# Kernel optimization log

Measured on AMD Instinct MI355X. Metric: run time of the kernel, lower is better.

## Reference

```python
import jax, jax.numpy as jnp
import numpy as np

B, S, E, H = 2, 2048, 1024, 16
D = E // H

def setup_inputs() -> dict:
    key = jax.random.key(0)
    ks = jax.random.split(key, 5)
    return {
        "hidden_states": jax.random.normal(ks[0], (B, S, E), dtype=jnp.float32),
        "c_attn_w": jax.random.normal(ks[1], (E, 3 * E), dtype=jnp.float32) * 0.02,
        "c_attn_b": jax.random.normal(ks[2], (3 * E,), dtype=jnp.float32) * 0.02,
        "c_proj_w": jax.random.normal(ks[3], (E, E), dtype=jnp.float32) * 0.02,
        "c_proj_b": jax.random.normal(ks[4], (E,), dtype=jnp.float32) * 0.02,
    }

def reference(hidden_states, c_attn_w, c_attn_b, c_proj_w, c_proj_b):
    x = hidden_states                      # [B, S, E]
    b, s, _ = x.shape
    w_q, w_k, w_v = jnp.split(c_attn_w, 3, axis=1)   # each [E, E]
    q_b, k_b, v_b = jnp.split(c_attn_b, 3, axis=0)   # each [E]

    # value projection
    v = x @ w_v + v_b                                        # [B,S,E]
    v = v.reshape(b, s, H, D).transpose(0, 2, 1, 3)          # [B,H,S,D]

    # fused query: ((x Wq + qb) Wk^T + kb)
    q = (x @ w_q + q_b) @ w_k.T + k_b                        # [B,S,E]
    qh = q.reshape(b, s, H, D).transpose(0, 2, 1, 3)         # [B,H,S,D]

    # key side is RAW hidden states split per head
    kh = x.reshape(b, s, H, D).transpose(0, 2, 1, 3)         # [B,H,S,D]

    scale = 1.0 / jnp.float32(D) ** 0.5
    scores = jnp.einsum("bhqd,bhkd->bhqk",
                        qh.astype(jnp.float32),
                        kh.astype(jnp.float32)) * scale       # [B,H,S,S] fp32

    causal = jnp.tril(jnp.ones((s, s), dtype=bool))
    mask_value = jnp.finfo(jnp.float32).min
    scores = jnp.where(causal[None, None], scores, mask_value)

    probs = jax.nn.softmax(scores, axis=-1).astype(v.dtype)  # [B,H,S,S]

    out = jnp.einsum("bhqk,bhkd->bhqd", probs, v)            # [B,H,S,D]
    out = out.transpose(0, 2, 1, 3).reshape(b, s, E)         # [B,S,E]
    out = out @ c_proj_w + c_proj_b
    return out
```

## Files before the change

kernel.cpp:

```cpp
#include <hip/hip_runtime.h>

typedef __attribute__((ext_vector_type(8))) __bf16 bf16x8;
typedef __attribute__((ext_vector_type(4))) __bf16 bf16x4;
typedef __attribute__((ext_vector_type(4))) float f32x4;

typedef __attribute__((address_space(1))) void as1_void;
typedef __attribute__((address_space(3))) void as3_void;

__device__ __forceinline__ void gl_lds16(const void* g, void* l) {
    __builtin_amdgcn_global_load_lds((const as1_void*)g, (as3_void*)l, 16, 0, 0);
}

__device__ __forceinline__ const bf16x8* swz(const __bf16* base, int row, int chunk) {
    return (const bf16x8*)((const char*)base + row * 128 + ((chunk ^ (row & 7)) * 16));
}

#define QSCALE (0.125f * 1.44269504f)

__global__ __launch_bounds__(256) void prep_kernel(
    const float* __restrict__ x, const float* __restrict__ caw,
    const float* __restrict__ cab, const float* __restrict__ cpw,
    __bf16* __restrict__ xb, __bf16* __restrict__ wvt,
    __bf16* __restrict__ wkn, __bf16* __restrict__ wqn,
    __bf16* __restrict__ wpt, float* __restrict__ bqv)
{
    __shared__ float tile[32 * 33];
    int bid = blockIdx.x;
    int tid = threadIdx.x;
    if (bid < 1024) {
        int nt = bid >> 5, kt = bid & 31;
        int tx = tid & 31, ty = tid >> 5;
        int n0 = nt * 32, k0 = kt * 32;
#pragma unroll
        for (int i = 0; i < 4; ++i)
            tile[(ty + i * 8) * 33 + tx] = caw[(long)(k0 + ty + i * 8) * 3072 + 2048 + n0 + tx];
        __syncthreads();
#pragma unroll
        for (int i = 0; i < 4; ++i)
            wvt[(long)(n0 + ty + i * 8) * 1024 + k0 + tx] = (__bf16)tile[tx * 33 + ty + i * 8];
    } else if (bid < 2048) {
        int v = bid - 1024;
        int nt = v >> 5, kt = v & 31;
        int tx = tid & 31, ty = tid >> 5;
        int n0 = nt * 32, k0 = kt * 32;
#pragma unroll
        for (int i = 0; i < 4; ++i)
            tile[(ty + i * 8) * 33 + tx] = cpw[(long)(k0 + ty + i * 8) * 1024 + n0 + tx];
        __syncthreads();
#pragma unroll
        for (int i = 0; i < 4; ++i)
            wpt[(long)(n0 + ty + i * 8) * 1024 + k0 + tx] = (__bf16)tile[tx * 33 + ty + i * 8];
    } else if (bid < 3072) {
        int e = (bid - 2048) * 1024 + tid * 4;
        int n = e >> 10, k = e & 1023;
        float4 f = *(const float4*)(caw + (long)n * 3072 + 1024 + k);
        bf16x4 o = {(__bf16)f.x, (__bf16)f.y, (__bf16)f.z, (__bf16)f.w};
        *(bf16x4*)(wkn + e) = o;
    } else if (bid < 4096) {
        int e = (bid - 3072) * 1024 + tid * 4;
        int n = e >> 10, k = e & 1023;
        float4 f = *(const float4*)(caw + (long)n * 3072 + k);
        bf16x4 o = {(__bf16)f.x, (__bf16)f.y, (__bf16)f.z, (__bf16)f.w};
        *(bf16x4*)(wqn + e) = o;
    } else if (bid < 8192) {
        long e = (long)(bid - 4096) * 1024 + tid * 4;
        float4 f = *(const float4*)(x + e);
        bf16x4 o = {(__bf16)f.x, (__bf16)f.y, (__bf16)f.z, (__bf16)f.w};
        *(bf16x4*)(xb + e) = o;
    } else {
        int k = bid - 8192;
        int wave = tid >> 6, lane = tid & 63;
        float qv[16];
#pragma unroll
        for (int u = 0; u < 4; ++u) {
            float4 q4 = *(const float4*)(cab + u * 256 + lane * 4);
            qv[u * 4 + 0] = q4.x; qv[u * 4 + 1] = q4.y;
            qv[u * 4 + 2] = q4.z; qv[u * 4 + 3] = q4.w;
        }
        for (int i = 0; i < 16; ++i) {
            int n = k * 64 + wave * 16 + i;
            float s = 0.f;
#pragma unroll
            for (int u = 0; u < 4; ++u) {
                float4 w4 = *(const float4*)(caw + (long)n * 3072 + 1024 + u * 256 + lane * 4);
                s += w4.x * qv[u * 4 + 0] + w4.y * qv[u * 4 + 1]
                   + w4.z * qv[u * 4 + 2] + w4.w * qv[u * 4 + 3];
            }
#pragma unroll
            for (int off = 1; off < 64; off <<= 1) s += __shfl_xor(s, off);
            if (lane == 0) bqv[n] = (s + cab[1024 + n]) * QSCALE;
        }
        if (tid < 64) bqv[1024 + k * 64 + tid] = cab[2048 + k * 64 + tid];
    }
}

template <bool BF16OUT, int BN>
__global__ __launch_bounds__(256) void gemm_bt(
    const __bf16* __restrict__ A, int lda,
    const __bf16* __restrict__ B, int ldb,
    const float* __restrict__ bias,
    void* __restrict__ C, int ldc, int K, float oscale)
{
    constexpr int NT = BN / 32;
    __shared__ __bf16 As[128 * 64];
    __shared__ __bf16 Bs[BN * 64];
    const int tid = threadIdx.x;
    const int lane = tid & 63;
    const int wave = tid >> 6;
    const int quad = lane >> 4, l16 = lane & 15;
    const long m0 = (long)blockIdx.y * 128;
    const long n0 = (long)blockIdx.x * BN;
    const int wm = (wave >> 1) * 64, wn = (wave & 1) * (BN / 2);

    f32x4 acc[4][NT] = {};

    for (int k0 = 0; k0 < K; k0 += 64) {
#pragma unroll
        for (int c = tid; c < (128 + BN) * 8; c += 256) {
            int row = c >> 3, cc = (c & 7) ^ (row & 7);
            if (row < 128)
                gl_lds16(A + (m0 + row) * lda + k0 + cc * 8, As + c * 8);
            else
                gl_lds16(B + (n0 + row - 128) * ldb + k0 + cc * 8, Bs + (c - 1024) * 8);
        }
        __syncthreads();
#pragma unroll
        for (int kk = 0; kk < 2; ++kk) {
            bf16x8 af[4], bfr[NT];
#pragma unroll
            for (int i = 0; i < 4; ++i)
                af[i] = *swz(As, wm + i * 16 + l16, kk * 4 + quad);
#pragma unroll
            for (int j = 0; j < NT; ++j)
                bfr[j] = *swz(Bs, wn + j * 16 + l16, kk * 4 + quad);
#pragma unroll
            for (int i = 0; i < 4; ++i)
#pragma unroll
                for (int j = 0; j < NT; ++j)
                    acc[i][j] = __builtin_amdgcn_mfma_f32_16x16x32_bf16(af[i], bfr[j], acc[i][j], 0, 0, 0);
        }
        __syncthreads();
    }
#pragma unroll
    for (int i = 0; i < 4; ++i) {
        long row = m0 + wm + i * 16 + quad * 4;
#pragma unroll
        for (int j = 0; j < NT; ++j) {
            int col = (int)n0 + wn + j * 16 + l16;
            float bb = bias ? bias[col] : 0.f;
#pragma unroll
            for (int r = 0; r < 4; ++r) {
                float v = (acc[i][j][r] + bb) * oscale;
                if (BF16OUT)
                    ((__bf16*)C)[(row + r) * ldc + col] = (__bf16)v;
                else
                    ((float*)C)[(row + r) * ldc + col] = v;
            }
        }
    }
}

__global__ __launch_bounds__(256) void gemm_qv(
    const __bf16* __restrict__ A,
    const __bf16* __restrict__ B,
    const float* __restrict__ bias,
    __bf16* __restrict__ Qout,
    __bf16* __restrict__ VTout)
{
    __shared__ __bf16 smem[128 * 136];
    __bf16* As = smem;
    __bf16* Bs = smem + 8192;
    const int tid = threadIdx.x;
    const int lane = tid & 63;
    const int wave = tid >> 6;
    const int quad = lane >> 4, l16 = lane & 15;
    const long m0 = (long)blockIdx.y * 128;
    const long n0 = (long)blockIdx.x * 128;
    const int wm = (wave >> 1) * 64, wn = (wave & 1) * 64;

    f32x4 acc[4][4] = {};

    for (int k0 = 0; k0 < 1024; k0 += 64) {
#pragma unroll
        for (int c = tid; c < 2048; c += 256) {
            int row = c >> 3, cc = (c & 7) ^ (row & 7);
            if (row < 128)
                gl_lds16(A + (m0 + row) * 1024 + k0 + cc * 8, As + c * 8);
            else
                gl_lds16(B + (n0 + row - 128) * 1024 + k0 + cc * 8, Bs + (c - 1024) * 8);
        }
        __syncthreads();
#pragma unroll
        for (int kk = 0; kk < 2; ++kk) {
            bf16x8 af[4], bfr[4];
#pragma unroll
            for (int i = 0; i < 4; ++i)
                af[i] = *swz(As, wm + i * 16 + l16, kk * 4 + quad);
#pragma unroll
            for (int j = 0; j < 4; ++j)
                bfr[j] = *swz(Bs, wn + j * 16 + l16, kk * 4 + quad);
#pragma unroll
            for (int i = 0; i < 4; ++i)
#pragma unroll
                for (int j = 0; j < 4; ++j)
                    acc[i][j] = __builtin_amdgcn_mfma_f32_16x16x32_bf16(af[i], bfr[j], acc[i][j], 0, 0, 0);
        }
        __syncthreads();
    }

    if (n0 < 1024) {
#pragma unroll
        for (int i = 0; i < 4; ++i) {
            long row = m0 + wm + i * 16 + quad * 4;
#pragma unroll
            for (int j = 0; j < 4; ++j) {
                int col = (int)n0 + wn + j * 16 + l16;
                float bb = bias[col];
#pragma unroll
                for (int r = 0; r < 4; ++r)
                    Qout[(row + r) * 1024 + col] = (__bf16)(acc[i][j][r] + bb);
            }
        }
    } else {
        __syncthreads();
#pragma unroll
        for (int i = 0; i < 4; ++i) {
#pragma unroll
            for (int j = 0; j < 4; ++j) {
                int col = (int)n0 + wn + j * 16 + l16;
                float bb = bias[col];
                bf16x4 v;
#pragma unroll
                for (int r = 0; r < 4; ++r) v[r] = (__bf16)(acc[i][j][r] + bb);
                *(bf16x4*)(smem + (wn + j * 16 + l16) * 136 + wm + i * 16 + quad * 4) = v;
            }
        }
        __syncthreads();
        const int d0 = (int)n0 - 1024;
        const int bb = (int)(m0 >> 11);
        const int sl = (int)(m0 & 2047);
#pragma unroll
        for (int pass = 0; pass < 16; ++pass) {
            int idx = pass * 256 + tid;
            int n = idx >> 5;
            int mc = (idx & 31) * 4;
            bf16x4 v = *(const bf16x4*)(smem + n * 136 + mc);
            *(bf16x4*)(VTout + ((long)(bb * 1024 + d0 + n)) * 2048 + sl + mc) = v;
        }
    }
}

__global__ __launch_bounds__(256, 2) void attn_kernel(
    const __bf16* __restrict__ Q,
    const __bf16* __restrict__ Xb,
    const __bf16* __restrict__ VT,
    __bf16* __restrict__ O)
{
    __shared__ __bf16 Ks[2 * 8192];
    __shared__ __bf16 Vs[2 * 8192];
    __shared__ __bf16 Ps[4 * 2048];
    const int tid = threadIdx.x;
    const int lane = tid & 63;
    const int wave = tid >> 6;
    const int group = wave >> 1;
    const int w2 = wave & 1;
    const int quad = lane >> 4, l16 = lane & 15;
    const int qa = blockIdx.y;
    const int qb = 31 - qa;
    const int qt = group ? qb : qa;
    const int bh = blockIdx.x;
    const int b = bh >> 4, h = bh & 15;
    const long rowbase = (long)b * 2048;

    const int i0 = tid, i1 = tid + 256;
    const int r0 = i0 >> 3, c0 = ((i0 & 7) ^ (r0 & 7)) * 8;
    const int r1 = i1 >> 3, c1 = ((i1 & 7) ^ (r1 & 7)) * 8;

    bf16x8 ones;
#pragma unroll
    for (int i = 0; i < 8; ++i) ones[i] = (__bf16)1.0f;

    bf16x8 qfr[2][2];
#pragma unroll
    for (int qg = 0; qg < 2; ++qg) {
        const __bf16* qp = Q + (rowbase + qt * 64 + w2 * 32 + qg * 16 + l16) * 1024 + h * 64 + quad * 8;
        qfr[qg][0] = *(const bf16x8*)(qp);
        qfr[qg][1] = *(const bf16x8*)(qp + 32);
    }

    const __bf16* kp0 = Xb + (rowbase + r0) * 1024 + h * 64 + c0;
    const __bf16* kp1 = Xb + (rowbase + r1) * 1024 + h * 64 + c1;
    const __bf16* vp0 = VT + ((long)(b * 1024 + h * 64 + r0)) * 2048 + c0;
    const __bf16* vp1 = VT + ((long)(b * 1024 + h * 64 + r1)) * 2048 + c1;

    auto stage_tile = [&](int j, int buf, int sub) {
        __bf16* kd = Ks + buf * 8192 + sub * 4096;
        __bf16* vd = Vs + buf * 8192 + sub * 4096;
        gl_lds16(kp0 + (long)j * 65536, kd + i0 * 8);
        gl_lds16(kp1 + (long)j * 65536, kd + i1 * 8);
        gl_lds16(vp0 + j * 64, vd + i0 * 8);
        gl_lds16(vp1 + j * 64, vd + i1 * 8);
    };
    stage_tile(0, 0, 0);
    stage_tile(1, 0, 1);

    const int nouter = (qb + 2) >> 1;

    f32x4 oacc[4][2] = {};
    f32x4 lacc[2] = {};
    __bf16* Pw = Ps + wave * 2048;

    for (int jj = 0; jj < nouter; ++jj) {
        __syncthreads();
        if (jj + 1 < nouter) {
            stage_tile(2 * jj + 2, (jj + 1) & 1, 0);
            stage_tile(2 * jj + 3, (jj + 1) & 1, 1);
        }

#pragma unroll
        for (int sub = 0; sub < 2; ++sub) {
            const int j = 2 * jj + sub;
            if (j > qt) continue;
            const __bf16* Kb = Ks + (jj & 1) * 8192 + sub * 4096;
            const __bf16* Vb = Vs + (jj & 1) * 8192 + sub * 4096;

            bf16x8 kf[2][4], vf[2][4];
#pragma unroll
            for (int kk = 0; kk < 2; ++kk)
#pragma unroll
                for (int kt = 0; kt < 4; ++kt) {
                    kf[kk][kt] = *swz(Kb, kt * 16 + l16, kk * 4 + quad);
                    vf[kk][kt] = *swz(Vb, kt * 16 + l16, kk * 4 + quad);
                }

            f32x4 sacc[4][2] = {};
#pragma unroll
            for (int kk = 0; kk < 2; ++kk)
#pragma unroll
                for (int kt = 0; kt < 4; ++kt)
#pragma unroll
                    for (int qg = 0; qg < 2; ++qg)
                        sacc[kt][qg] = __builtin_amdgcn_mfma_f32_16x16x32_bf16(
                            kf[kk][kt], qfr[qg][kk], sacc[kt][qg], 0, 0, 0);

            if (j == qt) {
#pragma unroll
                for (int kt = 0; kt < 4; ++kt)
#pragma unroll
                    for (int qg = 0; qg < 2; ++qg) {
                        const int qloc = w2 * 32 + qg * 16 + l16;
                        bf16x4 pk;
#pragma unroll
                        for (int r = 0; r < 4; ++r) {
                            float s = sacc[kt][qg][r];
                            if (kt * 16 + quad * 4 + r > qloc) s = -1e30f;
                            pk[r] = (__bf16)exp2f(s);
                        }
                        *(bf16x4*)((char*)Pw + (qg * 16 + l16) * 128 +
                                   (((kt * 2 + (quad >> 1)) ^ (l16 & 7)) * 16) + (quad & 1) * 8) = pk;
                    }
            } else {
#pragma unroll
                for (int kt = 0; kt < 4; ++kt)
#pragma unroll
                    for (int qg = 0; qg < 2; ++qg) {
                        bf16x4 pk;
#pragma unroll
                        for (int r = 0; r < 4; ++r)
                            pk[r] = (__bf16)exp2f(sacc[kt][qg][r]);
                        *(bf16x4*)((char*)Pw + (qg * 16 + l16) * 128 +
                                   (((kt * 2 + (quad >> 1)) ^ (l16 & 7)) * 16) + (quad & 1) * 8) = pk;
                    }
            }

#pragma unroll
            for (int kk = 0; kk < 2; ++kk) {
                bf16x8 pf[2];
#pragma unroll
                for (int qg = 0; qg < 2; ++qg) {
                    pf[qg] = *swz(Pw, qg * 16 + l16, kk * 4 + quad);
                    lacc[qg] = __builtin_amdgcn_mfma_f32_16x16x32_bf16(ones, pf[qg], lacc[qg], 0, 0, 0);
                }
#pragma unroll
                for (int dt = 0; dt < 4; ++dt)
#pragma unroll
                    for (int qg = 0; qg < 2; ++qg)
                        oacc[dt][qg] = __builtin_amdgcn_mfma_f32_16x16x32_bf16(
                            vf[kk][dt], pf[qg], oacc[dt][qg], 0, 0, 0);
            }
        }
    }

#pragma unroll
    for (int qg = 0; qg < 2; ++qg) {
        float inv = 1.0f / lacc[qg][0];
        long row = rowbase + qt * 64 + w2 * 32 + qg * 16 + l16;
#pragma unroll
        for (int dt = 0; dt < 4; ++dt) {
            bf16x4 ov;
#pragma unroll
            for (int r = 0; r < 4; ++r) ov[r] = (__bf16)(oacc[dt][qg][r] * inv);
            *(bf16x4*)(O + row * 1024 + h * 64 + dt * 16 + quad * 4) = ov;
        }
    }
}

extern "C" void kernel_launch(void* const* d_in, const int* in_sizes, int n_in,
                              void* d_out, int out_size, void* d_ws, size_t ws_size,
                              hipStream_t stream) {
    const float* x   = (const float*)d_in[0];
    const float* caw = (const float*)d_in[1];
    const float* cab = (const float*)d_in[2];
    const float* cpw = (const float*)d_in[3];
    const float* cpb = (const float*)d_in[4];

    char* p = (char*)d_ws;
    auto alloc = [&](size_t bytes) {
        void* r = (void*)p;
        p += (bytes + 255) & ~(size_t)255;
        return r;
    };
    __bf16* xb    = (__bf16*)alloc(4096UL * 1024 * 2);
    __bf16* mtb   = (__bf16*)alloc(1024UL * 1024 * 2);
    __bf16* wvt   = (__bf16*)alloc(1024UL * 1024 * 2);
    __bf16* wkn   = (__bf16*)alloc(1024UL * 1024 * 2);
    __bf16* wqn   = (__bf16*)alloc(1024UL * 1024 * 2);
    __bf16* wpt   = (__bf16*)alloc(1024UL * 1024 * 2);
    float*  bqv   = (float*) alloc(2048UL * 4);
    __bf16* qbuf  = (__bf16*)alloc(4096UL * 1024 * 2);
    __bf16* vt    = (__bf16*)alloc(2048UL * 2048 * 2);
    __bf16* attn  = (__bf16*)alloc(4096UL * 1024 * 2);

    prep_kernel<<<8208, 256, 0, stream>>>(x, caw, cab, cpw, xb, wvt, wkn, wqn, wpt, bqv);

    gemm_bt<true, 32><<<dim3(32, 8), 256, 0, stream>>>(wkn, 1024, wqn, 1024, nullptr,
                                                       (void*)mtb, 1024, 1024, QSCALE);
    gemm_qv<<<dim3(16, 32), 256, 0, stream>>>(xb, mtb, bqv, qbuf, vt);
    attn_kernel<<<dim3(32, 16), 256, 0, stream>>>(qbuf, xb, vt, attn);
    gemm_bt<false, 64><<<dim3(16, 32), 256, 0, stream>>>(attn, 1024, wpt, 1024, cpb,
                                                         d_out, 1024, 1024, 1.0f);
    (void)in_sizes; (void)n_in; (void)out_size; (void)ws_size;
}
```

Baseline: 191.8 us.

## Load V fragments directly from global memory and stage only K through LDS

The attention loop now processes one 64-key tile per iteration instead of two. Only K is double-buffered in LDS, while V fragments are read per wave straight from global memory into registers. The aim is to shrink LDS use and drop the V LDS round trip, with occupancy now left to the compiler by removing the launch-bounds minimum. The cost is that every wave issues its own global V loads, which duplicates traffic across waves, and those loads are exposed to memory latency with no prefetch. There is also one barrier per tile instead of one per two tiles.

```diff
diff --git a/kernel.cpp b/kernel.cpp
--- a/kernel.cpp
+++ b/kernel.cpp
@@ -250,14 +250,13 @@
     }
 }
 
-__global__ __launch_bounds__(256, 2) void attn_kernel(
+__global__ __launch_bounds__(256) void attn_kernel(
     const __bf16* __restrict__ Q,
     const __bf16* __restrict__ Xb,
     const __bf16* __restrict__ VT,
     __bf16* __restrict__ O)
 {
-    __shared__ __bf16 Ks[2 * 8192];
-    __shared__ __bf16 Vs[2 * 8192];
+    __shared__ __bf16 Ks[2 * 4096];
     __shared__ __bf16 Ps[4 * 2048];
     const int tid = threadIdx.x;
     const int lane = tid & 63;
@@ -290,104 +289,93 @@
 
     const __bf16* kp0 = Xb + (rowbase + r0) * 1024 + h * 64 + c0;
     const __bf16* kp1 = Xb + (rowbase + r1) * 1024 + h * 64 + c1;
-    const __bf16* vp0 = VT + ((long)(b * 1024 + h * 64 + r0)) * 2048 + c0;
-    const __bf16* vp1 = VT + ((long)(b * 1024 + h * 64 + r1)) * 2048 + c1;
-
-    auto stage_tile = [&](int j, int buf, int sub) {
-        __bf16* kd = Ks + buf * 8192 + sub * 4096;
-        __bf16* vd = Vs + buf * 8192 + sub * 4096;
+    const __bf16* vbase = VT + ((long)(b * 1024 + h * 64 + l16)) * 2048 + quad * 8;
+
+    auto stage_k = [&](int j, int buf) {
+        __bf16* kd = Ks + buf * 4096;
         gl_lds16(kp0 + (long)j * 65536, kd + i0 * 8);
         gl_lds16(kp1 + (long)j * 65536, kd + i1 * 8);
-        gl_lds16(vp0 + j * 64, vd + i0 * 8);
-        gl_lds16(vp1 + j * 64, vd + i1 * 8);
     };
-    stage_tile(0, 0, 0);
-    stage_tile(1, 0, 1);
-
-    const int nouter = (qb + 2) >> 1;
+    stage_k(0, 0);
 
     f32x4 oacc[4][2] = {};
     f32x4 lacc[2] = {};
     __bf16* Pw = Ps + wave * 2048;
 
-    for (int jj = 0; jj < nouter; ++jj) {
-        __syncthreads();
-        if (jj + 1 < nouter) {
-            stage_tile(2 * jj + 2, (jj + 1) & 1, 0);
-            stage_tile(2 * jj + 3, (jj + 1) & 1, 1);
-        }
-
-#pragma unroll
-        for (int sub = 0; sub < 2; ++sub) {
-            const int j = 2 * jj + sub;
-            if (j > qt) continue;
-            const __bf16* Kb = Ks + (jj & 1) * 8192 + sub * 4096;
-            const __bf16* Vb = Vs + (jj & 1) * 8192 + sub * 4096;
-
-            bf16x8 kf[2][4], vf[2][4];
-#pragma unroll
-            for (int kk = 0; kk < 2; ++kk)
-#pragma unroll
-                for (int kt = 0; kt < 4; ++kt) {
-                    kf[kk][kt] = *swz(Kb, kt * 16 + l16, kk * 4 + quad);
-                    vf[kk][kt] = *swz(Vb, kt * 16 + l16, kk * 4 + quad);
+    for (int j = 0; j <= qb; ++j) {
+        __syncthreads();
+        if (j < qb) stage_k(j + 1, (j + 1) & 1);
+        if (j > qt) continue;
+        const __bf16* Kb = Ks + (j & 1) * 4096;
+
+        bf16x8 vf[2][4];
+#pragma unroll
+        for (int kk = 0; kk < 2; ++kk)
+#pragma unroll
+            for (int dt = 0; dt < 4; ++dt)
+                vf[kk][dt] = *(const bf16x8*)(vbase + (long)dt * 32768 + j * 64 + kk * 32);
+
+        bf16x8 kf[2][4];
+#pragma unroll
+        for (int kk = 0; kk < 2; ++kk)
+#pragma unroll
+            for (int kt = 0; kt < 4; ++kt)
+                kf[kk][kt] = *swz(Kb, kt * 16 + l16, kk * 4 + quad);
+
+        f32x4 sacc[4][2] = {};
+#pragma unroll
+        for (int kk = 0; kk < 2; ++kk)
+#pragma unroll
+            for (int kt = 0; kt < 4; ++kt)
+#pragma unroll
+                for (int qg = 0; qg < 2; ++qg)
+                    sacc[kt][qg] = __builtin_amdgcn_mfma_f32_16x16x32_bf16(
+                        kf[kk][kt], qfr[qg][kk], sacc[kt][qg], 0, 0, 0);
+
+        if (j == qt) {
+#pragma unroll
+            for (int kt = 0; kt < 4; ++kt)
+#pragma unroll
+                for (int qg = 0; qg < 2; ++qg) {
+                    const int qloc = w2 * 32 + qg * 16 + l16;
+                    bf16x4 pk;
+#pragma unroll
+                    for (int r = 0; r < 4; ++r) {
+                        float s = sacc[kt][qg][r];
+                        if (kt * 16 + quad * 4 + r > qloc) s = -1e30f;
+                        pk[r] = (__bf16)exp2f(s);
+                    }
+                    *(bf16x4*)((char*)Pw + (qg * 16 + l16) * 128 +
+                               (((kt * 2 + (quad >> 1)) ^ (l16 & 7)) * 16) + (quad & 1) * 8) = pk;
                 }
-
-            f32x4 sacc[4][2] = {};
-#pragma unroll
-            for (int kk = 0; kk < 2; ++kk)
-#pragma unroll
-                for (int kt = 0; kt < 4; ++kt)
-#pragma unroll
-                    for (int qg = 0; qg < 2; ++qg)
-                        sacc[kt][qg] = __builtin_amdgcn_mfma_f32_16x16x32_bf16(
-                            kf[kk][kt], qfr[qg][kk], sacc[kt][qg], 0, 0, 0);
-
-            if (j == qt) {
-#pragma unroll
-                for (int kt = 0; kt < 4; ++kt)
-#pragma unroll
-                    for (int qg = 0; qg < 2; ++qg) {
-                        const int qloc = w2 * 32 + qg * 16 + l16;
-                        bf16x4 pk;
-#pragma unroll
-                        for (int r = 0; r < 4; ++r) {
-                            float s = sacc[kt][qg][r];
-                            if (kt * 16 + quad * 4 + r > qloc) s = -1e30f;
-                            pk[r] = (__bf16)exp2f(s);
-                        }
-                        *(bf16x4*)((char*)Pw + (qg * 16 + l16) * 128 +
-                                   (((kt * 2 + (quad >> 1)) ^ (l16 & 7)) * 16) + (quad & 1) * 8) = pk;
-                    }
-            } else {
-#pragma unroll
-                for (int kt = 0; kt < 4; ++kt)
-#pragma unroll
-                    for (int qg = 0; qg < 2; ++qg) {
-                        bf16x4 pk;
-#pragma unroll
-                        for (int r = 0; r < 4; ++r)
-                            pk[r] = (__bf16)exp2f(sacc[kt][qg][r]);
-                        *(bf16x4*)((char*)Pw + (qg * 16 + l16) * 128 +
-                                   (((kt * 2 + (quad >> 1)) ^ (l16 & 7)) * 16) + (quad & 1) * 8) = pk;
-                    }
+        } else {
+#pragma unroll
+            for (int kt = 0; kt < 4; ++kt)
+#pragma unroll
+                for (int qg = 0; qg < 2; ++qg) {
+                    bf16x4 pk;
+#pragma unroll
+                    for (int r = 0; r < 4; ++r)
+                        pk[r] = (__bf16)exp2f(sacc[kt][qg][r]);
+                    *(bf16x4*)((char*)Pw + (qg * 16 + l16) * 128 +
+                               (((kt * 2 + (quad >> 1)) ^ (l16 & 7)) * 16) + (quad & 1) * 8) = pk;
+                }
+        }
+
+#pragma unroll
+        for (int kk = 0; kk < 2; ++kk) {
+            bf16x8 pf[2];
+#pragma unroll
+            for (int qg = 0; qg < 2; ++qg) {
+                pf[qg] = *swz(Pw, qg * 16 + l16, kk * 4 + quad);
+                lacc[qg] = __builtin_amdgcn_mfma_f32_16x16x32_bf16(ones, pf[qg], lacc[qg], 0, 0, 0);
             }
-
-#pragma unroll
-            for (int kk = 0; kk < 2; ++kk) {
-                bf16x8 pf[2];
-#pragma unroll
-                for (int qg = 0; qg < 2; ++qg) {
-                    pf[qg] = *swz(Pw, qg * 16 + l16, kk * 4 + quad);
-                    lacc[qg] = __builtin_amdgcn_mfma_f32_16x16x32_bf16(ones, pf[qg], lacc[qg], 0, 0, 0);
-                }
-#pragma unroll
-                for (int dt = 0; dt < 4; ++dt)
-#pragma unroll
-                    for (int qg = 0; qg < 2; ++qg)
-                        oacc[dt][qg] = __builtin_amdgcn_mfma_f32_16x16x32_bf16(
-                            vf[kk][dt], pf[qg], oacc[dt][qg], 0, 0, 0);
-            }
+#pragma unroll
+            for (int dt = 0; dt < 4; ++dt)
+#pragma unroll
+                for (int qg = 0; qg < 2; ++qg)
+                    oacc[dt][qg] = __builtin_amdgcn_mfma_f32_16x16x32_bf16(
+                        vf[kk][dt], pf[qg], oacc[dt][qg], 0, 0, 0);
         }
     }
 
```

New measurement: 203.1 us. 5.9% more time.
